# Optimization experiments

Measured on AMD Instinct MI355X. Metric: run time of the kernel, lower is better.

The kernel has to match this reference:

```python
import jax, jax.numpy as jnp
import numpy as np

BS = 512          # batch size
S = 63            # max_sequence_length = 32 leaves + 31 reduces
D = 256           # feature_dim == word_dim
VD = 512          # visual_dim
R = 196           # num_region (14x14)
VOCAB = 50257     # word_number
NOUT = 3000       # num_output


def setup_inputs() -> dict:
    key = jax.random.key(0)
    ks = jax.random.split(key, 24)
    u = lambda k, shp: jax.random.uniform(k, shp, jnp.float32, -0.01, 0.01)
    # valid shift-reduce program: push,push,(reduce,push)*30,reduce  (left-deep tree)
    row = np.array([0, 0] + [1, 0] * 30 + [1], dtype=np.int64)
    assert row.shape[0] == S
    ops = jnp.asarray(np.tile(row, (BS, 1)))
    return {
        "v": jax.random.normal(ks[0], (BS, R, VD), jnp.float32),
        "questions": jax.random.randint(ks[1], (BS, S), 0, VOCAB),
        "ops": ops,
        "bs": BS,
        "wembed": jax.random.uniform(ks[2], (VOCAB, D), jnp.float32, -1.0, 1.0),
        "W_w": u(ks[3], (D, VD)), "W_b": jnp.zeros((D,), jnp.float32),
        "Wi_w": u(ks[4], (D, D)), "Wi_b": jnp.zeros((D,), jnp.float32),
        "Wu_w": u(ks[5], (D, D)), "Wu_b": jnp.zeros((D,), jnp.float32),
        "Wo_w": u(ks[6], (D, D)), "Wo_b": jnp.zeros((D,), jnp.float32),
        "Ui_w": u(ks[7], (D, D)), "Ui_b": jnp.zeros((D,), jnp.float32),
        "Uf_w": u(ks[8], (D, D)), "Uf_b": jnp.ones((D,), jnp.float32),
        "Uo_w": u(ks[9], (D, D)), "Uo_b": jnp.zeros((D,), jnp.float32),
        "Uu_w": u(ks[10], (D, D)), "Uu_b": jnp.zeros((D,), jnp.float32),
        "WQ_w": u(ks[11], (D, D)), "WQ_b": jnp.zeros((D,), jnp.float32),
        "WV_w": u(ks[12], (D, D)),
        "WP_w": u(ks[13], (1, D)), "WP_b": jnp.zeros((1,), jnp.float32),
        "FC1_w": u(ks[14], (D, D)), "FC1_b": jnp.zeros((D,), jnp.float32),
        "FC2_w": u(ks[15], (NOUT, D)), "FC2_b": jnp.zeros((NOUT,), jnp.float32),
    }


def _forward(v, questions, ops, wembed, W_w, W_b, Wi_w, Wi_b, Wu_w, Wu_b,
             Wo_w, Wo_b, Ui_w, Ui_b, Uf_w, Uf_b, Uo_w, Uo_b, Uu_w, Uu_b,
             WQ_w, WQ_b, WV_w, WP_w, WP_b, FC1_w, FC1_b, FC2_w, FC2_b):
    B, Sl = questions.shape
    Dm = W_w.shape[0]
    # visual projection: [B, R, VD] -> [B, R, D]
    vv = jnp.tanh(jnp.einsum('brv,dv->brd', v, W_w) + W_b)
    # leaf states from word embeddings
    q = wembed[questions]                                   # [B, S, D]
    ig = jax.nn.sigmoid(jnp.einsum('bsd,ed->bse', q, Wi_w) + Wi_b)
    ug = jnp.tanh(jnp.einsum('bsd,ed->bse', q, Wu_w) + Wu_b)
    og = jax.nn.sigmoid(jnp.einsum('bsd,ed->bse', q, Wo_w) + Wo_b)
    buff_c = ig * ug
    buff_h = og * jnp.tanh(buff_c)
    # stack-based shift-reduce TreeLSTM, vectorized over the batch
    bidx = jnp.arange(B)
    stack_h = jnp.zeros((B, Sl + 2, Dm), q.dtype)
    stack_c = jnp.zeros((B, Sl + 2, Dm), q.dtype)
    ptr = jnp.zeros((B,), jnp.int32)

    def step(carry, x):
        sh, sc, ptr = carry
        bh, bc, op = x                                      # [B,D],[B,D],[B]
        r_idx = jnp.maximum(ptr - 1, 0)
        l_idx = jnp.maximum(ptr - 2, 0)
        h2, c2 = sh[bidx, r_idx], sc[bidx, r_idx]           # right child
        h1, c1 = sh[bidx, l_idx], sc[bidx, l_idx]           # left child
        hsum = h1 + h2
        i_g = jax.nn.sigmoid(hsum @ Ui_w.T + Ui_b)
        o_g = jax.nn.sigmoid(hsum @ Uo_w.T + Uo_b)
        u_g = jnp.tanh(hsum @ Uu_w.T + Uu_b)
        f1 = jax.nn.sigmoid(h1 @ Uf_w.T + Uf_b)
        f2 = jax.nn.sigmoid(h2 @ Uf_w.T + Uf_b)
        c_new = i_g * u_g + f1 * c1 + f2 * c2
        h_new = o_g * jnp.tanh(c_new)
        is_push = (op == 0)[:, None]
        is_red = (op == 1)[:, None]
        widx = jnp.where(op == 0, ptr, l_idx)               # push at top, reduce writes left slot
        val_h = jnp.where(is_push, bh, jnp.where(is_red, h_new, sh[bidx, widx]))
        val_c = jnp.where(is_push, bc, jnp.where(is_red, c_new, sc[bidx, widx]))
        sh = sh.at[bidx, widx].set(val_h)
        sc = sc.at[bidx, widx].set(val_c)
        ptr = ptr + jnp.where(op == 0, 1, jnp.where(op == 1, -1, 0)).astype(ptr.dtype)
        return (sh, sc, ptr), None

    xs = (jnp.swapaxes(buff_h, 0, 1), jnp.swapaxes(buff_c, 0, 1), ops.T)
    (stack_h, stack_c, ptr), _ = jax.lax.scan(step, (stack_h, stack_c, ptr), xs)
    r = stack_h[bidx, jnp.maximum(ptr - 1, 0)]              # [B, D] final root h
    # attention over image regions (additive form, use_mult=False)
    wvi = jnp.einsum('brd,ed->bre', vv, WV_w)               # [B, R, D]
    wqq = (r @ WQ_w.T + WQ_b)[:, None, :]                   # [B, 1, D]
    hA = jnp.tanh(wqq + wvi)
    scores = jnp.einsum('brd,od->bro', hA, WP_w)[..., 0] + WP_b[0]  # [B, R]
    p = jax.nn.softmax(scores, axis=-1)
    att = jnp.einsum('br,brd->bd', p, vv) + r
    # two_fc classifier head
    return jnp.tanh(att @ FC1_w.T + FC1_b) @ FC2_w.T + FC2_b


def reference(v, questions, ops, bs, wembed, W_w, W_b, Wi_w, Wi_b, Wu_w, Wu_b,
              Wo_w, Wo_b, Ui_w, Ui_b, Uf_w, Uf_b, Uo_w, Uo_b, Uu_w, Uu_b,
              WQ_w, WQ_b, WV_w, WP_w, WP_b, FC1_w, FC1_b, FC2_w, FC2_b):
    del bs  # batch size implied by array shapes
    return _forward(v, questions, ops, wembed, W_w, W_b, Wi_w, Wi_b, Wu_w, Wu_b,
                    Wo_w, Wo_b, Ui_w, Ui_b, Uf_w, Uf_b, Uo_w, Uo_b, Uu_w, Uu_b,
                    WQ_w, WQ_b, WV_w, WP_w, WP_b, FC1_w, FC1_b, FC2_w, FC2_b)
```

## Files before the change

### kernel.cpp

```cpp
#include <hip/hip_runtime.h>
#include <hip/hip_bf16.h>

#define BSZ   512
#define SEQ   63
#define DIM   256
#define VDIM  512
#define RREG  196
#define NOUTP 3000

using f32x4_t  = __attribute__((ext_vector_type(4))) float;
using bf16x8_t = __attribute__((ext_vector_type(8))) short;

__device__ inline float bf2f(unsigned short u){
  union { unsigned int i; float f; } x; x.i = ((unsigned int)u) << 16; return x.f;
}
__device__ inline unsigned short f2bf(float f){
  unsigned int u = __float_as_uint(f);
  unsigned int r = (u + 0x7fffu + ((u >> 16) & 1u)) >> 16;
  return (unsigned short)r;
}
__device__ inline unsigned int bfpack(float a, float b){
  return (unsigned int)f2bf(a) | ((unsigned int)f2bf(b) << 16);
}
__device__ inline void bf2x(unsigned int w, float& a, float& b){
  union { unsigned int i; float f; } x, y;
  x.i = w << 16; y.i = w & 0xffff0000u; a = x.f; b = y.f;
}
__device__ inline float sigm(float x){ return 1.f / (1.f + __expf(-x)); }
__device__ inline float ftanh(float x){ return 1.f - 2.f / (__expf(2.f * x) + 1.f); }

__device__ inline f32x4_t mfma16(bf16x8_t a, bf16x8_t b, f32x4_t c){
  return __builtin_amdgcn_mfma_f32_16x16x32_bf16(a, b, c, 0, 0, 0);
}

#define OFF_WWBF   0u
#define OFF_WIBF   262144u
#define OFF_WUBF   393216u
#define OFF_WOBF   524288u
#define OFF_UIBF   655360u
#define OFF_UFBF   786432u
#define OFF_UOBF   917504u
#define OFF_UUBF   1048576u
#define OFF_WVBF   1179648u
#define OFF_WQBF   1310720u
#define OFF_FC1BF  1441792u
#define OFF_FC2BF  1572864u
#define OFF_RVEC   3112960u
#define OFF_Z      3637248u
#define OFF_BH     4161536u
#define OFF_BC     20676608u

struct ConvArgs {
  const float* src[13];
  unsigned short* dst[13];
  int n[13];
};

__global__ __launch_bounds__(256) void k0_convert(ConvArgs a){
  const int gid = blockIdx.x * 256 + threadIdx.x;
  const int stride = gridDim.x * 256;
  #pragma unroll 1
  for (int j = 0; j < 13; ++j){
    const float* s = a.src[j];
    unsigned short* d = a.dst[j];
    const int n = a.n[j];
    if (s){
      for (int i = gid; i < n; i += stride) d[i] = f2bf(s[i]);
    } else {
      for (int i = gid; i < n; i += stride) d[i] = 0;
    }
  }
}

__global__ __launch_bounds__(256) void k1_leaf(
    const int* __restrict__ questions, const float* __restrict__ wembed,
    const unsigned short* __restrict__ Wi, const unsigned short* __restrict__ Wu,
    const unsigned short* __restrict__ Wo,
    const float* __restrict__ Wib, const float* __restrict__ Wub, const float* __restrict__ Wob,
    unsigned short* __restrict__ bh, unsigned short* __restrict__ bc)
{
  __shared__ unsigned short qt[64][264];
  __shared__ int qidx[64];
  const int tid = threadIdx.x;
  const int row0 = blockIdx.x * 64;
  if (tid < 64) qidx[tid] = questions[row0 + tid];
  __syncthreads();
  {
    const int mb = tid >> 4, c = (tid & 15) * 16;
    #pragma unroll
    for (int rr = 0; rr < 4; ++rr){
      const int m = mb + rr * 16;
      const float* src = wembed + (size_t)qidx[m] * DIM + c;
      #pragma unroll
      for (int k = 0; k < 16; k += 4){
        float4 x = *(const float4*)(src + k);
        *(unsigned int*)&qt[m][c + k]     = bfpack(x.x, x.y);
        *(unsigned int*)&qt[m][c + k + 2] = bfpack(x.z, x.w);
      }
    }
  }
  __syncthreads();
  const int lane = tid & 63, wv = tid >> 6;
  const int lr = lane & 15, lk = (lane >> 4) * 8;
  for (int et = 0; et < 4; ++et){
    const int e = et * 64 + wv * 16 + lr;
    bf16x8_t Bi[8], Bu[8], Bo[8];
    const size_t wb = (size_t)e * DIM + lk;
    #pragma unroll
    for (int kk = 0; kk < 8; ++kk){
      Bi[kk] = *(const bf16x8_t*)(Wi + wb + kk * 32);
      Bu[kk] = *(const bf16x8_t*)(Wu + wb + kk * 32);
      Bo[kk] = *(const bf16x8_t*)(Wo + wb + kk * 32);
    }
    const float bi = Wib[e], bu = Wub[e], bo = Wob[e];
    for (int mt = 0; mt < 4; ++mt){
      f32x4_t ai = {0,0,0,0}, au = {0,0,0,0}, ao = {0,0,0,0};
      const unsigned short* ar = &qt[mt * 16 + lr][lk];
      #pragma unroll
      for (int kk = 0; kk < 8; ++kk){
        bf16x8_t A = *(const bf16x8_t*)(ar + kk * 32);
        ai = mfma16(A, Bi[kk], ai);
        au = mfma16(A, Bu[kk], au);
        ao = mfma16(A, Bo[kk], ao);
      }
      #pragma unroll
      for (int j = 0; j < 4; ++j){
        const int m = mt * 16 + (lane >> 4) * 4 + j;
        const float ig = sigm(ai[j] + bi), ug = ftanh(au[j] + bu), og = sigm(ao[j] + bo);
        const float cc = ig * ug, hh = og * ftanh(cc);
        const size_t o = (size_t)(row0 + m) * DIM + e;
        bc[o] = f2bf(cc); bh[o] = f2bf(hh);
      }
    }
  }
}

#define LSLOTS 4
#define HSLOT  4224
__global__ __launch_bounds__(512) void k2_tree(
    const int* __restrict__ ops,
    const unsigned short* __restrict__ bh, const unsigned short* __restrict__ bc,
    const unsigned short* __restrict__ Ui, const unsigned short* __restrict__ Uf,
    const unsigned short* __restrict__ Uo, const unsigned short* __restrict__ Uu,
    const float* __restrict__ Uib, const float* __restrict__ Ufb,
    const float* __restrict__ Uob, const float* __restrict__ Uub,
    float* __restrict__ r_vec)
{
  __shared__ unsigned short hstk[LSLOTS * HSLOT];
  __shared__ float          cstk[LSLOTS * HSLOT];
  __shared__ unsigned short HSb[HSLOT];
  __shared__ float          rtop[HSLOT];
  __shared__ int opm[16], ptrv[16], lidxA[16], ridxA[16];

  const int tid = threadIdx.x;
  const int lane = tid & 63, wv = tid >> 6;
  const int lr = lane & 15, lk = (lane >> 4) * 8;
  const int rb = blockIdx.x * 16;

  for (int i = tid; i < LSLOTS * HSLOT / 8; i += 512) ((uint4*)hstk)[i] = uint4{0,0,0,0};
  for (int i = tid; i < LSLOTS * HSLOT / 4; i += 512) ((uint4*)cstk)[i] = uint4{0,0,0,0};
  for (int i = tid; i < HSLOT / 8;          i += 512) ((uint4*)HSb)[i]  = uint4{0,0,0,0};
  for (int i = tid; i < HSLOT / 4;          i += 512) ((uint4*)rtop)[i] = uint4{0,0,0,0};
  if (tid < 16) ptrv[tid] = 0;

  float bI[2], bO[2], bU[2], bF[2];
  int eo[2];
  #pragma unroll
  for (int et = 0; et < 2; ++et){
    const int e = wv * 32 + et * 16 + lr;
    eo[et] = e; bI[et] = Uib[e]; bO[et] = Uob[e]; bU[et] = Uub[e]; bF[et] = Ufb[e];
  }

  const int pm = tid >> 5, pc = (tid & 31) * 8;
  bf16x8_t ph  = *(const bf16x8_t*)(bh + ((size_t)(rb + pm) * SEQ + 0) * DIM + pc);
  bf16x8_t pcv = *(const bf16x8_t*)(bc + ((size_t)(rb + pm) * SEQ + 0) * DIM + pc);

  __syncthreads();

  for (int s = 0; s < SEQ; ++s){
    if (tid < 16){
      opm[tid] = ops[(size_t)(rb + tid) * SEQ + s];
      const int p = ptrv[tid];
      lidxA[tid] = (p - 2 > 0) ? (p - 2) : 0;
      ridxA[tid] = (p - 1 > 0) ? (p - 1) : 0;
    }
    __syncthreads();
    bool anyred = false, anypush = false;
    #pragma unroll
    for (int m = 0; m < 16; ++m){ const int o = opm[m]; anyred |= (o == 1); anypush |= (o == 0); }

    if (anypush && opm[pm] == 0){
      const int ps = (ptrv[pm] < LSLOTS - 1) ? ptrv[pm] : (LSLOTS - 1);
      *(bf16x8_t*)(hstk + ps * HSLOT + pm * 264 + pc) = ph;
      float cf[8];
      #pragma unroll
      for (int i = 0; i < 8; ++i) cf[i] = bf2f((unsigned short)pcv[i]);
      float* cd = cstk + ps * HSLOT + pm * 264 + pc;
      *(float4*)(cd)     = float4{cf[0], cf[1], cf[2], cf[3]};
      *(float4*)(cd + 4) = float4{cf[4], cf[5], cf[6], cf[7]};
      float* rd = rtop + pm * 264 + pc;
      #pragma unroll
      for (int i = 0; i < 8; ++i) rd[i] = bf2f((unsigned short)ph[i]);
    }
    if (anyred && opm[pm] == 1){
      const int sl = lidxA[pm], sr = ridxA[pm];
      bf16x8_t a8 = *(const bf16x8_t*)(hstk + sl * HSLOT + pm * 264 + pc);
      bf16x8_t b8 = *(const bf16x8_t*)(hstk + sr * HSLOT + pm * 264 + pc);
      unsigned int* hd = (unsigned int*)(HSb + pm * 264 + pc);
      #pragma unroll
      for (int i = 0; i < 4; ++i){
        const float s0 = bf2f((unsigned short)a8[2*i])   + bf2f((unsigned short)b8[2*i]);
        const float s1 = bf2f((unsigned short)a8[2*i+1]) + bf2f((unsigned short)b8[2*i+1]);
        hd[i] = bfpack(s0, s1);
      }
    }
    if (s + 1 < SEQ){
      ph  = *(const bf16x8_t*)(bh + ((size_t)(rb + pm) * SEQ + (s + 1)) * DIM + pc);
      pcv = *(const bf16x8_t*)(bc + ((size_t)(rb + pm) * SEQ + (s + 1)) * DIM + pc);
    }

    if (anyred){
      __syncthreads();
      float hnv[2][4], cnv[2][4];
      const int sl1 = lidxA[lr], sl2 = ridxA[lr];
      const unsigned short* pS = HSb + lr * 264 + lk;
      const unsigned short* p1 = hstk + sl1 * HSLOT + lr * 264 + lk;
      const unsigned short* p2 = hstk + sl2 * HSLOT + lr * 264 + lk;
      #pragma unroll
      for (int et = 0; et < 2; ++et){
        const int e = eo[et];
        const size_t wb = (size_t)e * DIM + lk;
        f32x4_t ai = {0,0,0,0}, ao = {0,0,0,0}, au = {0,0,0,0}, a1 = {0,0,0,0}, a2 = {0,0,0,0};
        #pragma unroll
        for (int kk = 0; kk < 8; ++kk){
          bf16x8_t AS = *(const bf16x8_t*)(pS + kk * 32);
          bf16x8_t A1 = *(const bf16x8_t*)(p1 + kk * 32);
          bf16x8_t A2 = *(const bf16x8_t*)(p2 + kk * 32);
          bf16x8_t Wi_ = *(const bf16x8_t*)(Ui + wb + kk * 32);
          bf16x8_t Wo_ = *(const bf16x8_t*)(Uo + wb + kk * 32);
          bf16x8_t Wu_ = *(const bf16x8_t*)(Uu + wb + kk * 32);
          bf16x8_t Wf_ = *(const bf16x8_t*)(Uf + wb + kk * 32);
          ai = mfma16(AS, Wi_, ai);
          ao = mfma16(AS, Wo_, ao);
          au = mfma16(AS, Wu_, au);
          a1 = mfma16(A1, Wf_, a1);
          a2 = mfma16(A2, Wf_, a2);
        }
        #pragma unroll
        for (int j = 0; j < 4; ++j){
          const int m = (lane >> 4) * 4 + j;
          const float ig = sigm(ai[j] + bI[et]), og = sigm(ao[j] + bO[et]), ug = ftanh(au[j] + bU[et]);
          const float f1 = sigm(a1[j] + bF[et]), f2 = sigm(a2[j] + bF[et]);
          const float c1 = cstk[lidxA[m] * HSLOT + m * 264 + e];
          const float c2 = cstk[ridxA[m] * HSLOT + m * 264 + e];
          const float cn = ig * ug + f1 * c1 + f2 * c2;
          cnv[et][j] = cn;
          hnv[et][j] = og * ftanh(cn);
        }
      }
      __syncthreads();
      #pragma unroll
      for (int et = 0; et < 2; ++et){
        #pragma unroll
        for (int j = 0; j < 4; ++j){
          const int m = (lane >> 4) * 4 + j;
          if (opm[m] == 1){
            const int sl = lidxA[m];
            hstk[sl * HSLOT + m * 264 + eo[et]] = f2bf(hnv[et][j]);
            cstk[sl * HSLOT + m * 264 + eo[et]] = cnv[et][j];
            rtop[m * 264 + eo[et]] = hnv[et][j];
          }
        }
      }
      if (tid < 16){
        const int o = opm[tid];
        ptrv[tid] += (o == 0) ? 1 : ((o == 1) ? -1 : 0);
      }
      __syncthreads();
    } else {
      __syncthreads();
      if (tid < 16){
        const int o = opm[tid];
        ptrv[tid] += (o == 0) ? 1 : ((o == 1) ? -1 : 0);
      }
    }
  }
  __syncthreads();
  {
    const float* rs = rtop + pm * 264 + pc;
    float* dst = r_vec + (size_t)(rb + pm) * DIM + pc;
    *(float4*)(dst)     = *(const float4*)(rs);
    *(float4*)(dst + 4) = *(const float4*)(rs + 4);
  }
}

__global__ __launch_bounds__(256) void k34_attn(
    const float* __restrict__ v, const unsigned short* __restrict__ Wwbf,
    const float* __restrict__ W_b, const float* __restrict__ r_vec,
    const unsigned short* __restrict__ WQbf, const float* __restrict__ WQb,
    const unsigned short* __restrict__ WVbf, const float* __restrict__ WPw,
    const unsigned short* __restrict__ FC1bf, const float* __restrict__ FC1b,
    float* __restrict__ z)
{
  __shared__ unsigned short vvt[196 * 264];
  __shared__ char sun[16896];
  __shared__ float scv[216];
  __shared__ float wqv[256];
  __shared__ float rld[256];
  __shared__ float attv[256];
  __shared__ float wpld[256];
  __shared__ float red[8];
  unsigned short* vstage = (unsigned short*)sun;
  float* pre = (float*)sun;

  const int b = blockIdx.x, tid = threadIdx.x;
  const int lane = tid & 63, wv = tid >> 6;
  const int lr = lane & 15, lk = (lane >> 4) * 8;

  rld[tid]  = r_vec[(size_t)b * DIM + tid];
  wpld[tid] = WPw[tid];

  bf16x8_t Aw[4][16];
  float wbias[4];
  #pragma unroll
  for (int et = 0; et < 4; ++et){
    const int e = et * 64 + wv * 16 + lr;
    wbias[et] = W_b[e];
    const size_t wb = (size_t)e * VDIM + lk;
    #pragma unroll
    for (int kk = 0; kk < 16; ++kk) Aw[et][kk] = *(const bf16x8_t*)(Wwbf + wb + kk * 32);
  }
  __syncthreads();
  {
    float acc = WQb[tid];
    const unsigned short* wr = WQbf + (size_t)tid * DIM;
    for (int d = 0; d < DIM; d += 8){
      uint4 w4 = *(const uint4*)(wr + d);
      float a0,a1,a2,a3,a4,a5,a6,a7;
      bf2x(w4.x,a0,a1); bf2x(w4.y,a2,a3); bf2x(w4.z,a4,a5); bf2x(w4.w,a6,a7);
      acc += a0*rld[d] + a1*rld[d+1] + a2*rld[d+2] + a3*rld[d+3]
           + a4*rld[d+4] + a5*rld[d+5] + a6*rld[d+6] + a7*rld[d+7];
    }
    wqv[tid] = acc;
  }
  for (int t = 0; t < 13; ++t){
    const int r0 = t * 16;
    __syncthreads();
    {
      const int m = tid >> 4, c = (tid & 15) * 32;
      const int gr = r0 + m;
      if (gr < RREG){
        const float* src = v + ((size_t)b * RREG + gr) * VDIM + c;
        #pragma unroll
        for (int k = 0; k < 32; k += 4){
          float4 x = *(const float4*)(src + k);
          *(unsigned int*)&vstage[m * 520 + c + k]     = bfpack(x.x, x.y);
          *(unsigned int*)&vstage[m * 520 + c + k + 2] = bfpack(x.z, x.w);
        }
      }
    }
    __syncthreads();
    #pragma unroll
    for (int et = 0; et < 4; ++et){
      const int e = et * 64 + wv * 16 + lr;
      f32x4_t acc = {0,0,0,0};
      const unsigned short* ar = vstage + lr * 520 + lk;
      #pragma unroll
      for (int kk = 0; kk < 16; ++kk)
        acc = mfma16(*(const bf16x8_t*)(ar + kk * 32), Aw[et][kk], acc);
      #pragma unroll
      for (int j = 0; j < 4; ++j){
        const int gr = r0 + (lane >> 4) * 4 + j;
        if (gr < RREG) vvt[gr * 264 + e] = f2bf(ftanh(acc[j] + wbias[et]));
      }
    }
  }
  bf16x8_t Bv[4][8];
  #pragma unroll
  for (int et = 0; et < 4; ++et){
    const int e = et * 64 + wv * 16 + lr;
    const size_t wb = (size_t)e * DIM + lk;
    #pragma unroll
    for (int kk = 0; kk < 8; ++kk) Bv[et][kk] = *(const bf16x8_t*)(WVbf + wb + kk * 32);
  }
  __syncthreads();
  for (int t = 0; t < 13; ++t){
    const int arow = t * 16 + lr;
    const unsigned short* ar = vvt + ((arow < RREG) ? arow : (RREG - 1)) * 264 + lk;
    #pragma unroll
    for (int et = 0; et < 4; ++et){
      const int e = et * 64 + wv * 16 + lr;
      f32x4_t acc = {0,0,0,0};
      #pragma unroll
      for (int kk = 0; kk < 8; ++kk)
        acc = mfma16(*(const bf16x8_t*)(ar + kk * 32), Bv[et][kk], acc);
      const float wqe = wqv[e];
      #pragma unroll
      for (int j = 0; j < 4; ++j){
        const int m = (lane >> 4) * 4 + j;
        pre[m * 264 + e] = ftanh(acc[j] + wqe);
      }
    }
    __syncthreads();
    {
      const int m = tid >> 4, cc = (tid & 15) * 16;
      float p_ = 0.f;
      #pragma unroll
      for (int k = 0; k < 16; ++k) p_ += pre[m * 264 + cc + k] * wpld[cc + k];
      #pragma unroll
      for (int off = 8; off; off >>= 1) p_ += __shfl_xor(p_, off, 16);
      if ((tid & 15) == 0){
        const int rr = t * 16 + m;
        scv[rr] = (rr < RREG) ? p_ : -1e30f;
      }
    }
    __syncthreads();
  }
  {
    const float sv = (tid < RREG) ? scv[tid] : -1e30f;
    float m_ = sv;
    #pragma unroll
    for (int off = 32; off; off >>= 1) m_ = fmaxf(m_, __shfl_xor(m_, off, 64));
    if (lane == 0) red[wv] = m_;
    __syncthreads();
    m_ = fmaxf(fmaxf(red[0], red[1]), fmaxf(red[2], red[3]));
    const float ex = (tid < RREG) ? __expf(sv - m_) : 0.f;
    float s_ = ex;
    #pragma unroll
    for (int off = 32; off; off >>= 1) s_ += __shfl_xor(s_, off, 64);
    if (lane == 0) red[4 + wv] = s_;
    __syncthreads();
    s_ = red[4] + red[5] + red[6] + red[7];
    if (tid < RREG) scv[tid] = ex / s_;
  }
  __syncthreads();
  {
    float a = rld[tid];
    #pragma unroll 4
    for (int rr = 0; rr < RREG; ++rr) a += scv[rr] * bf2f(vvt[rr * 264 + tid]);
    attv[tid] = a;
  }
  __syncthreads();
  {
    float acc = FC1b[tid];
    const unsigned short* wr = FC1bf + (size_t)tid * DIM;
    for (int d = 0; d < DIM; d += 8){
      uint4 w4 = *(const uint4*)(wr + d);
      float a0,a1,a2,a3,a4,a5,a6,a7;
      bf2x(w4.x,a0,a1); bf2x(w4.y,a2,a3); bf2x(w4.z,a4,a5); bf2x(w4.w,a6,a7);
      acc += a0*attv[d] + a1*attv[d+1] + a2*attv[d+2] + a3*attv[d+3]
           + a4*attv[d+4] + a5*attv[d+5] + a6*attv[d+6] + a7*attv[d+7];
    }
    z[(size_t)b * DIM + tid] = ftanh(acc);
  }
}

__global__ __launch_bounds__(256) void k5_fc2(
    const float* __restrict__ z, const unsigned short* __restrict__ FC2bf,
    const float* __restrict__ FC2b, float* __restrict__ out)
{
  __shared__ unsigned short zt[16][264];
  const int tid = threadIdx.x;
  const int rb = blockIdx.x * 16, ob = blockIdx.y * 64;
  {
    const int m = tid >> 4, c = (tid & 15) * 16;
    const float* src = z + (size_t)(rb + m) * DIM + c;
    #pragma unroll
    for (int k = 0; k < 16; k += 4){
      float4 x = *(const float4*)(src + k);
      *(unsigned int*)&zt[m][c + k]     = bfpack(x.x, x.y);
      *(unsigned int*)&zt[m][c + k + 2] = bfpack(x.z, x.w);
    }
  }
  __syncthreads();
  const int lane = tid & 63, wv = tid >> 6;
  const int lr = lane & 15, lk = (lane >> 4) * 8;
  const int o = ob + wv * 16 + lr;
  f32x4_t acc = {0,0,0,0};
  const size_t wb = (size_t)o * DIM + lk;
  const unsigned short* ar = &zt[lr][lk];
  #pragma unroll
  for (int kk = 0; kk < 8; ++kk){
    bf16x8_t A = *(const bf16x8_t*)(ar + kk * 32);
    bf16x8_t Bb = *(const bf16x8_t*)(FC2bf + wb + kk * 32);
    acc = mfma16(A, Bb, acc);
  }
  if (o < NOUTP){
    const float bo = FC2b[o];
    #pragma unroll
    for (int j = 0; j < 4; ++j){
      const int m = (lane >> 4) * 4 + j;
      out[(size_t)(rb + m) * NOUTP + o] = acc[j] + bo;
    }
  }
}

extern "C" void kernel_launch(void* const* d_in, const int* in_sizes, int n_in,
                              void* d_out, int out_size, void* d_ws, size_t ws_size,
                              hipStream_t stream) {
  const float* v         = (const float*)d_in[0];
  const int*   questions = (const int*)d_in[1];
  const int*   ops       = (const int*)d_in[2];
  const float* wembed    = (const float*)d_in[4];
  const float* W_w  = (const float*)d_in[5];   const float* W_b  = (const float*)d_in[6];
  const float* Wi_w = (const float*)d_in[7];   const float* Wi_b = (const float*)d_in[8];
  const float* Wu_w = (const float*)d_in[9];   const float* Wu_b = (const float*)d_in[10];
  const float* Wo_w = (const float*)d_in[11];  const float* Wo_b = (const float*)d_in[12];
  const float* Ui_w = (const float*)d_in[13];  const float* Ui_b = (const float*)d_in[14];
  const float* Uf_w = (const float*)d_in[15];  const float* Uf_b = (const float*)d_in[16];
  const float* Uo_w = (const float*)d_in[17];  const float* Uo_b = (const float*)d_in[18];
  const float* Uu_w = (const float*)d_in[19];  const float* Uu_b = (const float*)d_in[20];
  const float* WQ_w = (const float*)d_in[21];  const float* WQ_b = (const float*)d_in[22];
  const float* WV_w = (const float*)d_in[23];
  const float* WP_w = (const float*)d_in[24];
  const float* FC1_w = (const float*)d_in[26]; const float* FC1_b = (const float*)d_in[27];
  const float* FC2_w = (const float*)d_in[28]; const float* FC2_b = (const float*)d_in[29];
  float* out = (float*)d_out;
  char* ws = (char*)d_ws;

  unsigned short* Wwbf  = (unsigned short*)(ws + OFF_WWBF);
  unsigned short* Wibf  = (unsigned short*)(ws + OFF_WIBF);
  unsigned short* Wubf  = (unsigned short*)(ws + OFF_WUBF);
  unsigned short* Wobf  = (unsigned short*)(ws + OFF_WOBF);
  unsigned short* Uibf  = (unsigned short*)(ws + OFF_UIBF);
  unsigned short* Ufbf  = (unsigned short*)(ws + OFF_UFBF);
  unsigned short* Uobf  = (unsigned short*)(ws + OFF_UOBF);
  unsigned short* Uubf  = (unsigned short*)(ws + OFF_UUBF);
  unsigned short* WVbf  = (unsigned short*)(ws + OFF_WVBF);
  unsigned short* WQbf  = (unsigned short*)(ws + OFF_WQBF);
  unsigned short* FC1bf = (unsigned short*)(ws + OFF_FC1BF);
  unsigned short* FC2bf = (unsigned short*)(ws + OFF_FC2BF);
  float* r_vec = (float*)(ws + OFF_RVEC);
  float* z     = (float*)(ws + OFF_Z);
  unsigned short* bh = (unsigned short*)(ws + OFF_BH);
  unsigned short* bc = (unsigned short*)(ws + OFF_BC);

  ConvArgs ca;
  const float* srcs[13] = { W_w, Wi_w, Wu_w, Wo_w, Ui_w, Uf_w, Uo_w, Uu_w, WV_w, WQ_w, FC1_w, FC2_w, nullptr };
  unsigned short* dsts[13] = { Wwbf, Wibf, Wubf, Wobf, Uibf, Ufbf, Uobf, Uubf, WVbf, WQbf, FC1bf, FC2bf, FC2bf + 768000 };
  int ns[13] = { 131072, 65536, 65536, 65536, 65536, 65536, 65536, 65536, 65536, 65536, 65536, 768000, 2048 };
  for (int i = 0; i < 13; ++i){ ca.src[i] = srcs[i]; ca.dst[i] = dsts[i]; ca.n[i] = ns[i]; }
  k0_convert<<<512, 256, 0, stream>>>(ca);

  k1_leaf<<<504, 256, 0, stream>>>(questions, wembed, Wibf, Wubf, Wobf, Wi_b, Wu_b, Wo_b, bh, bc);

  k2_tree<<<32, 512, 0, stream>>>(ops, bh, bc, Uibf, Ufbf, Uobf, Uubf,
                                  Ui_b, Uf_b, Uo_b, Uu_b, r_vec);

  k34_attn<<<512, 256, 0, stream>>>(v, Wwbf, W_b, r_vec, WQbf, WQ_b, WVbf, WP_w,
                                    FC1bf, FC1_b, z);

  k5_fc2<<<dim3(32, 47), 256, 0, stream>>>(z, FC2bf, FC2_b, out);

  (void)in_sizes; (void)n_in; (void)out_size; (void)ws_size;
}
```

Baseline: 1.127 ms.

## Widen tree kernel to 1024 threads, precompute stack schedule, double-buffer visual staging

The tree-LSTM kernel now runs 1024 threads per block, each wave owning 16 output features instead of 32. All shift/reduce ops, stack indices and per-step reduce flags are precomputed into shared memory up front. This drops the per-step op loading, pointer updates and one barrier per step. The attention kernel double-buffers the visual-region staging so global loads for the next 16 rows overlap the MFMA for the current rows, at the cost of more shared memory. Risks are higher register pressure under the new launch bounds and lower occupancy from the larger LDS footprint.

```diff
diff --git a/kernel.cpp b/kernel.cpp
--- a/kernel.cpp
+++ b/kernel.cpp
@@ -10,6 +10,7 @@
 
 using f32x4_t  = __attribute__((ext_vector_type(4))) float;
 using bf16x8_t = __attribute__((ext_vector_type(8))) short;
+using u16x4_t  = __attribute__((ext_vector_type(4))) unsigned short;
 
 __device__ inline float bf2f(unsigned short u){
   union { unsigned int i; float f; } x; x.i = ((unsigned int)u) << 16; return x.f;
@@ -137,7 +138,7 @@
 
 #define LSLOTS 4
 #define HSLOT  4224
-__global__ __launch_bounds__(512) void k2_tree(
+__global__ __launch_bounds__(1024, 4) void k2_tree(
     const int* __restrict__ ops,
     const unsigned short* __restrict__ bh, const unsigned short* __restrict__ bc,
     const unsigned short* __restrict__ Ui, const unsigned short* __restrict__ Uf,
@@ -150,147 +151,139 @@
   __shared__ float          cstk[LSLOTS * HSLOT];
   __shared__ unsigned short HSb[HSLOT];
   __shared__ float          rtop[HSLOT];
-  __shared__ int opm[16], ptrv[16], lidxA[16], ridxA[16];
+  __shared__ unsigned char stOp[SEQ][16], stL[SEQ][16], stR[SEQ][16], stW[SEQ][16];
+  __shared__ unsigned char stRed[SEQ];
 
   const int tid = threadIdx.x;
-  const int lane = tid & 63, wv = tid >> 6;
+  const int lane = tid & 63;
+  const int wv = tid >> 6;
   const int lr = lane & 15, lk = (lane >> 4) * 8;
   const int rb = blockIdx.x * 16;
-
-  for (int i = tid; i < LSLOTS * HSLOT / 8; i += 512) ((uint4*)hstk)[i] = uint4{0,0,0,0};
-  for (int i = tid; i < LSLOTS * HSLOT / 4; i += 512) ((uint4*)cstk)[i] = uint4{0,0,0,0};
-  for (int i = tid; i < HSLOT / 8;          i += 512) ((uint4*)HSb)[i]  = uint4{0,0,0,0};
-  for (int i = tid; i < HSLOT / 4;          i += 512) ((uint4*)rtop)[i] = uint4{0,0,0,0};
-  if (tid < 16) ptrv[tid] = 0;
-
-  float bI[2], bO[2], bU[2], bF[2];
-  int eo[2];
-  #pragma unroll
-  for (int et = 0; et < 2; ++et){
-    const int e = wv * 32 + et * 16 + lr;
-    eo[et] = e; bI[et] = Uib[e]; bO[et] = Uob[e]; bU[et] = Uub[e]; bF[et] = Ufb[e];
-  }
-
-  const int pm = tid >> 5, pc = (tid & 31) * 8;
-  bf16x8_t ph  = *(const bf16x8_t*)(bh + ((size_t)(rb + pm) * SEQ + 0) * DIM + pc);
-  bf16x8_t pcv = *(const bf16x8_t*)(bc + ((size_t)(rb + pm) * SEQ + 0) * DIM + pc);
-
+  const int e  = wv * 16 + lr;
+  const int pm = wv;
+  const int pc = lane * 4;
+
+  for (int i = tid; i < LSLOTS * HSLOT / 8; i += 1024) ((uint4*)hstk)[i] = uint4{0,0,0,0};
+  for (int i = tid; i < LSLOTS * HSLOT / 4; i += 1024) ((uint4*)cstk)[i] = uint4{0,0,0,0};
+  for (int i = tid; i < HSLOT / 8;          i += 1024) ((uint4*)HSb)[i]  = uint4{0,0,0,0};
+  for (int i = tid; i < HSLOT / 4;          i += 1024) ((uint4*)rtop)[i] = uint4{0,0,0,0};
+  if (tid < SEQ * 16){
+    const int m = tid & 15, s = tid >> 4;
+    stOp[s][m] = (unsigned char)ops[(size_t)(rb + m) * SEQ + s];
+  }
+  __syncthreads();
+  if (tid < 16){
+    int p = 0;
+    for (int s = 0; s < SEQ; ++s){
+      const int o = stOp[s][tid];
+      const int l = (p - 2 > 0) ? (p - 2) : 0;
+      const int r = (p - 1 > 0) ? (p - 1) : 0;
+      stL[s][tid] = (unsigned char)l;
+      stR[s][tid] = (unsigned char)r;
+      stW[s][tid] = (unsigned char)((o == 0) ? ((p < LSLOTS - 1) ? p : (LSLOTS - 1)) : l);
+      p += (o == 0) ? 1 : ((o == 1) ? -1 : 0);
+    }
+  } else if (tid >= 64 && tid < 64 + SEQ){
+    const int s = tid - 64;
+    int any = 0;
+    #pragma unroll
+    for (int m = 0; m < 16; ++m) any |= (stOp[s][m] == 1) ? 1 : 0;
+    stRed[s] = (unsigned char)any;
+  }
+
+  const float bI = Uib[e], bO = Uob[e], bU = Uub[e], bF = Ufb[e];
+  u16x4_t ph  = *(const u16x4_t*)(bh + ((size_t)(rb + pm) * SEQ + 0) * DIM + pc);
+  u16x4_t pcv = *(const u16x4_t*)(bc + ((size_t)(rb + pm) * SEQ + 0) * DIM + pc);
   __syncthreads();
 
   for (int s = 0; s < SEQ; ++s){
-    if (tid < 16){
-      opm[tid] = ops[(size_t)(rb + tid) * SEQ + s];
-      const int p = ptrv[tid];
-      lidxA[tid] = (p - 2 > 0) ? (p - 2) : 0;
-      ridxA[tid] = (p - 1 > 0) ? (p - 1) : 0;
-    }
-    __syncthreads();
-    bool anyred = false, anypush = false;
-    #pragma unroll
-    for (int m = 0; m < 16; ++m){ const int o = opm[m]; anyred |= (o == 1); anypush |= (o == 0); }
-
-    if (anypush && opm[pm] == 0){
-      const int ps = (ptrv[pm] < LSLOTS - 1) ? ptrv[pm] : (LSLOTS - 1);
-      *(bf16x8_t*)(hstk + ps * HSLOT + pm * 264 + pc) = ph;
-      float cf[8];
-      #pragma unroll
-      for (int i = 0; i < 8; ++i) cf[i] = bf2f((unsigned short)pcv[i]);
-      float* cd = cstk + ps * HSLOT + pm * 264 + pc;
-      *(float4*)(cd)     = float4{cf[0], cf[1], cf[2], cf[3]};
-      *(float4*)(cd + 4) = float4{cf[4], cf[5], cf[6], cf[7]};
-      float* rd = rtop + pm * 264 + pc;
-      #pragma unroll
-      for (int i = 0; i < 8; ++i) rd[i] = bf2f((unsigned short)ph[i]);
-    }
-    if (anyred && opm[pm] == 1){
-      const int sl = lidxA[pm], sr = ridxA[pm];
-      bf16x8_t a8 = *(const bf16x8_t*)(hstk + sl * HSLOT + pm * 264 + pc);
-      bf16x8_t b8 = *(const bf16x8_t*)(hstk + sr * HSLOT + pm * 264 + pc);
-      unsigned int* hd = (unsigned int*)(HSb + pm * 264 + pc);
-      #pragma unroll
-      for (int i = 0; i < 4; ++i){
-        const float s0 = bf2f((unsigned short)a8[2*i])   + bf2f((unsigned short)b8[2*i]);
-        const float s1 = bf2f((unsigned short)a8[2*i+1]) + bf2f((unsigned short)b8[2*i+1]);
-        hd[i] = bfpack(s0, s1);
-      }
+    const int myop = stOp[s][pm];
+    if (myop == 0){
+      const int ps = stW[s][pm];
+      *(u16x4_t*)(hstk + ps * HSLOT + pm * 264 + pc) = ph;
+      float4 cf = { bf2f((unsigned short)pcv[0]), bf2f((unsigned short)pcv[1]),
+                    bf2f((unsigned short)pcv[2]), bf2f((unsigned short)pcv[3]) };
+      *(float4*)(cstk + ps * HSLOT + pm * 264 + pc) = cf;
+      float4 hf = { bf2f((unsigned short)ph[0]), bf2f((unsigned short)ph[1]),
+                    bf2f((unsigned short)ph[2]), bf2f((unsigned short)ph[3]) };
+      *(float4*)(rtop + pm * 264 + pc) = hf;
+    } else {
+      const int sl = stL[s][pm], sr = stR[s][pm];
+      u16x4_t a4 = *(const u16x4_t*)(hstk + sl * HSLOT + pm * 264 + pc);
+      u16x4_t b4 = *(const u16x4_t*)(hstk + sr * HSLOT + pm * 264 + pc);
+      u16x4_t o4;
+      #pragma unroll
+      for (int i = 0; i < 4; ++i)
+        o4[i] = f2bf(bf2f((unsigned short)a4[i]) + bf2f((unsigned short)b4[i]));
+      *(u16x4_t*)(HSb + pm * 264 + pc) = o4;
     }
     if (s + 1 < SEQ){
-      ph  = *(const bf16x8_t*)(bh + ((size_t)(rb + pm) * SEQ + (s + 1)) * DIM + pc);
-      pcv = *(const bf16x8_t*)(bc + ((size_t)(rb + pm) * SEQ + (s + 1)) * DIM + pc);
-    }
-
-    if (anyred){
+      ph  = *(const u16x4_t*)(bh + ((size_t)(rb + pm) * SEQ + (s + 1)) * DIM + pc);
+      pcv = *(const u16x4_t*)(bc + ((size_t)(rb + pm) * SEQ + (s + 1)) * DIM + pc);
+    }
+
+    if (stRed[s]){
       __syncthreads();
-      float hnv[2][4], cnv[2][4];
-      const int sl1 = lidxA[lr], sl2 = ridxA[lr];
-      const unsigned short* pS = HSb + lr * 264 + lk;
+      const int sl1 = stL[s][lr], sl2 = stR[s][lr];
       const unsigned short* p1 = hstk + sl1 * HSLOT + lr * 264 + lk;
       const unsigned short* p2 = hstk + sl2 * HSLOT + lr * 264 + lk;
-      #pragma unroll
-      for (int et = 0; et < 2; ++et){
-        const int e = eo[et];
-        const size_t wb = (size_t)e * DIM + lk;
-        f32x4_t ai = {0,0,0,0}, ao = {0,0,0,0}, au = {0,0,0,0}, a1 = {0,0,0,0}, a2 = {0,0,0,0};
+      const unsigned short* pS = HSb + lr * 264 + lk;
+      bf16x8_t AS[8];
+      #pragma unroll
+      for (int kk = 0; kk < 8; ++kk) AS[kk] = *(const bf16x8_t*)(pS + kk * 32);
+      const size_t wb = (size_t)e * DIM + lk;
+      f32x4_t ai = {0,0,0,0}, ao = {0,0,0,0}, au = {0,0,0,0}, a1 = {0,0,0,0}, a2 = {0,0,0,0};
+      {
+        bf16x8_t wf[8];
+        #pragma unroll
+        for (int kk = 0; kk < 8; ++kk) wf[kk] = *(const bf16x8_t*)(Ui + wb + kk * 32);
+        #pragma unroll
+        for (int kk = 0; kk < 8; ++kk) ai = mfma16(AS[kk], wf[kk], ai);
+        #pragma unroll
+        for (int kk = 0; kk < 8; ++kk) wf[kk] = *(const bf16x8_t*)(Uo + wb + kk * 32);
+        #pragma unroll
+        for (int kk = 0; kk < 8; ++kk) ao = mfma16(AS[kk], wf[kk], ao);
+        #pragma unroll
+        for (int kk = 0; kk < 8; ++kk) wf[kk] = *(const bf16x8_t*)(Uu + wb + kk * 32);
+        #pragma unroll
+        for (int kk = 0; kk < 8; ++kk) au = mfma16(AS[kk], wf[kk], au);
+        #pragma unroll
+        for (int kk = 0; kk < 8; ++kk) wf[kk] = *(const bf16x8_t*)(Uf + wb + kk * 32);
         #pragma unroll
         for (int kk = 0; kk < 8; ++kk){
-          bf16x8_t AS = *(const bf16x8_t*)(pS + kk * 32);
-          bf16x8_t A1 = *(const bf16x8_t*)(p1 + kk * 32);
-          bf16x8_t A2 = *(const bf16x8_t*)(p2 + kk * 32);
-          bf16x8_t Wi_ = *(const bf16x8_t*)(Ui + wb + kk * 32);
-          bf16x8_t Wo_ = *(const bf16x8_t*)(Uo + wb + kk * 32);
-          bf16x8_t Wu_ = *(const bf16x8_t*)(Uu + wb + kk * 32);
-          bf16x8_t Wf_ = *(const bf16x8_t*)(Uf + wb + kk * 32);
-          ai = mfma16(AS, Wi_, ai);
-          ao = mfma16(AS, Wo_, ao);
-          au = mfma16(AS, Wu_, au);
-          a1 = mfma16(A1, Wf_, a1);
-          a2 = mfma16(A2, Wf_, a2);
+          a1 = mfma16(*(const bf16x8_t*)(p1 + kk * 32), wf[kk], a1);
+          a2 = mfma16(*(const bf16x8_t*)(p2 + kk * 32), wf[kk], a2);
         }
-        #pragma unroll
-        for (int j = 0; j < 4; ++j){
-          const int m = (lane >> 4) * 4 + j;
-          const float ig = sigm(ai[j] + bI[et]), og = sigm(ao[j] + bO[et]), ug = ftanh(au[j] + bU[et]);
-          const float f1 = sigm(a1[j] + bF[et]), f2 = sigm(a2[j] + bF[et]);
-          const float c1 = cstk[lidxA[m] * HSLOT + m * 264 + e];
-          const float c2 = cstk[ridxA[m] * HSLOT + m * 264 + e];
-          const float cn = ig * ug + f1 * c1 + f2 * c2;
-          cnv[et][j] = cn;
-          hnv[et][j] = og * ftanh(cn);
+      }
+      float hn[4], cn[4];
+      #pragma unroll
+      for (int j = 0; j < 4; ++j){
+        const int m = (lane >> 4) * 4 + j;
+        const float ig = sigm(ai[j] + bI), og = sigm(ao[j] + bO), ug = ftanh(au[j] + bU);
+        const float f1 = sigm(a1[j] + bF), f2 = sigm(a2[j] + bF);
+        const float c1 = cstk[(int)stL[s][m] * HSLOT + m * 264 + e];
+        const float c2 = cstk[(int)stR[s][m] * HSLOT + m * 264 + e];
+        cn[j] = ig * ug + f1 * c1 + f2 * c2;
+        hn[j] = og * ftanh(cn[j]);
+      }
+      __syncthreads();
+      #pragma unroll
+      for (int j = 0; j < 4; ++j){
+        const int m = (lane >> 4) * 4 + j;
+        if (stOp[s][m] == 1){
+          const int sl = stL[s][m];
+          hstk[sl * HSLOT + m * 264 + e] = f2bf(hn[j]);
+          cstk[sl * HSLOT + m * 264 + e] = cn[j];
+          rtop[m * 264 + e] = hn[j];
         }
       }
       __syncthreads();
-      #pragma unroll
-      for (int et = 0; et < 2; ++et){
-        #pragma unroll
-        for (int j = 0; j < 4; ++j){
-          const int m = (lane >> 4) * 4 + j;
-          if (opm[m] == 1){
-            const int sl = lidxA[m];
-            hstk[sl * HSLOT + m * 264 + eo[et]] = f2bf(hnv[et][j]);
-            cstk[sl * HSLOT + m * 264 + eo[et]] = cnv[et][j];
-            rtop[m * 264 + eo[et]] = hnv[et][j];
-          }
-        }
-      }
-      if (tid < 16){
-        const int o = opm[tid];
-        ptrv[tid] += (o == 0) ? 1 : ((o == 1) ? -1 : 0);
-      }
-      __syncthreads();
-    } else {
-      __syncthreads();
-      if (tid < 16){
-        const int o = opm[tid];
-        ptrv[tid] += (o == 0) ? 1 : ((o == 1) ? -1 : 0);
-      }
     }
   }
   __syncthreads();
   {
     const float* rs = rtop + pm * 264 + pc;
-    float* dst = r_vec + (size_t)(rb + pm) * DIM + pc;
-    *(float4*)(dst)     = *(const float4*)(rs);
-    *(float4*)(dst + 4) = *(const float4*)(rs + 4);
+    *(float4*)(r_vec + (size_t)(rb + pm) * DIM + pc) = *(const float4*)(rs);
   }
 }
 
@@ -303,7 +296,7 @@
     float* __restrict__ z)
 {
   __shared__ unsigned short vvt[196 * 264];
-  __shared__ char sun[16896];
+  __shared__ char sun[33280];
   __shared__ float scv[216];
   __shared__ float wqv[256];
   __shared__ float rld[256];
@@ -330,7 +323,6 @@
     #pragma unroll
     for (int kk = 0; kk < 16; ++kk) Aw[et][kk] = *(const bf16x8_t*)(Wwbf + wb + kk * 32);
   }
-  __syncthreads();
   {
     float acc = WQb[tid];
     const unsigned short* wr = WQbf + (size_t)tid * DIM;
@@ -343,35 +335,50 @@
     }
     wqv[tid] = acc;
   }
-  for (int t = 0; t < 13; ++t){
-    const int r0 = t * 16;
-    __syncthreads();
+  {
+    float4 xr[8];
+    const int sm = tid >> 4, sc = (tid & 15) * 32;
     {
-      const int m = tid >> 4, c = (tid & 15) * 32;
-      const int gr = r0 + m;
-      if (gr < RREG){
-        const float* src = v + ((size_t)b * RREG + gr) * VDIM + c;
-        #pragma unroll
-        for (int k = 0; k < 32; k += 4){
-          float4 x = *(const float4*)(src + k);
-          *(unsigned int*)&vstage[m * 520 + c + k]     = bfpack(x.x, x.y);
-          *(unsigned int*)&vstage[m * 520 + c + k + 2] = bfpack(x.z, x.w);
+      const float* src = v + ((size_t)b * RREG + sm) * VDIM + sc;
+      #pragma unroll
+      for (int k = 0; k < 8; ++k) xr[k] = *(const float4*)(src + k * 4);
+      unsigned short* dst = vstage + sm * 520 + sc;
+      #pragma unroll
+      for (int k = 0; k < 8; ++k){
+        *(unsigned int*)(dst + k * 4)     = bfpack(xr[k].x, xr[k].y);
+        *(unsigned int*)(dst + k * 4 + 2) = bfpack(xr[k].z, xr[k].w);
+      }
+    }
+    for (int t = 0; t < 13; ++t){
+      __syncthreads();
+      const int gr = (t + 1) * 16 + sm;
+      if (t < 12 && gr < RREG){
+        const float* src = v + ((size_t)b * RREG + gr) * VDIM + sc;
+        #pragma unroll
+        for (int k = 0; k < 8; ++k) xr[k] = *(const float4*)(src + k * 4);
+      }
+      const unsigned short* bufc = vstage + (t & 1) * 8320;
+      #pragma unroll
+      for (int et = 0; et < 4; ++et){
+        const int e = et * 64 + wv * 16 + lr;
+        f32x4_t acc = {0,0,0,0};
+        const unsigned short* ar = bufc + lr * 520 + lk;
+        #pragma unroll
+        for (int kk = 0; kk < 16; ++kk)
+          acc = mfma16(*(const bf16x8_t*)(ar + kk * 32), Aw[et][kk], acc);
+        #pragma unroll
+        for (int j = 0; j < 4; ++j){
+          const int orow = t * 16 + (lane >> 4) * 4 + j;
+          if (orow < RREG) vvt[orow * 264 + e] = f2bf(ftanh(acc[j] + wbias[et]));
         }
       }
-    }
-    __syncthreads();
-    #pragma unroll
-    for (int et = 0; et < 4; ++et){
-      const int e = et * 64 + wv * 16 + lr;
-      f32x4_t acc = {0,0,0,0};
-      const unsigned short* ar = vstage + lr * 520 + lk;
-      #pragma unroll
-      for (int kk = 0; kk < 16; ++kk)
-        acc = mfma16(*(const bf16x8_t*)(ar + kk * 32), Aw[et][kk], acc);
-      #pragma unroll
-      for (int j = 0; j < 4; ++j){
-        const int gr = r0 + (lane >> 4) * 4 + j;
-        if (gr < RREG) vvt[gr * 264 + e] = f2bf(ftanh(acc[j] + wbias[et]));
+      if (t < 12){
+        unsigned short* dst = vstage + ((t + 1) & 1) * 8320 + sm * 520 + sc;
+        #pragma unroll
+        for (int k = 0; k < 8; ++k){
+          *(unsigned int*)(dst + k * 4)     = bfpack(xr[k].x, xr[k].y);
+          *(unsigned int*)(dst + k * 4 + 2) = bfpack(xr[k].z, xr[k].w);
+        }
       }
     }
   }
@@ -544,8 +551,8 @@
 
   k1_leaf<<<504, 256, 0, stream>>>(questions, wembed, Wibf, Wubf, Wobf, Wi_b, Wu_b, Wo_b, bh, bc);
 
-  k2_tree<<<32, 512, 0, stream>>>(ops, bh, bc, Uibf, Ufbf, Uobf, Uubf,
-                                  Ui_b, Uf_b, Uo_b, Uu_b, r_vec);
+  k2_tree<<<32, 1024, 0, stream>>>(ops, bh, bc, Uibf, Ufbf, Uobf, Uubf,
+                                   Ui_b, Uf_b, Uo_b, Uu_b, r_vec);
 
   k34_attn<<<512, 256, 0, stream>>>(v, Wwbf, W_b, r_vec, WQbf, WQ_b, WVbf, WP_w,
                                     FC1bf, FC1_b, z);
```

New measurement: 1.076 ms. -4.5%, faster.
